# Optimization experiments

Measured on AMD Instinct MI355X. Metric: run time of the kernel, lower is better.

The kernel has to match this reference:

```python
import jax, jax.numpy as jnp
import numpy as np

C, C_LO, C_MF = 96, 32, 32  # c_hf = 96 - 32 - 32 = 32
K_LO, K_HI, LP_FINE, LP_COARSE = 5, 3, 3, 7
BN_EPS = 1e-5


def _avgpool_same(x, k):
    """AvgPool2d(k, stride=1, padding=k//2, count_include_pad=False) on NCHW."""
    p = k // 2
    dims, strides = (1, 1, k, k), (1, 1, 1, 1)
    pads = ((0, 0), (0, 0), (p, p), (p, p))
    s = jax.lax.reduce_window(x, jnp.float32(0), jax.lax.add, dims, strides, pads)
    ones = jnp.ones((1, 1) + x.shape[2:], x.dtype)
    cnt = jax.lax.reduce_window(ones, jnp.float32(0), jax.lax.add, dims, strides, pads)
    return s / cnt  # divide by number of VALID (non-pad) elements


def _dwconv(x, w, k):
    """Depthwise conv, 'same' padding, no bias. w: (C, 1, k, k)."""
    p = k // 2
    return jax.lax.conv_general_dilated(
        x, w, window_strides=(1, 1), padding=((p, p), (p, p)),
        dimension_numbers=("NCHW", "OIHW", "NCHW"),
        feature_group_count=x.shape[1])


def setup_inputs() -> dict:
    key = jax.random.key(0)
    ks = jax.random.split(key, 8)
    B, H, W = 8, 256, 256
    return {
        "x": jax.random.normal(ks[0], (B, C, H, W), jnp.float32),
        "w_lo": jax.random.normal(ks[1], (C_LO, 1, K_LO, K_LO), jnp.float32) * 0.1,
        "w_mf": jax.random.normal(ks[2], (C_MF, 1, 3, 3), jnp.float32) * 0.2,
        "w_hf": jax.random.normal(ks[3], (C - C_LO - C_MF, 1, K_HI, K_HI), jnp.float32) * 0.2,
        "bn_gamma": jax.random.uniform(ks[4], (C,), jnp.float32, 0.5, 1.5),
        "bn_beta": jax.random.normal(ks[5], (C,), jnp.float32) * 0.1,
        "bn_mean": jax.random.normal(ks[6], (C,), jnp.float32) * 0.1,
        "bn_var": jax.random.uniform(ks[7], (C,), jnp.float32, 0.5, 1.5),
    }


def reference(x, w_lo, w_mf, w_hf, bn_gamma, bn_beta, bn_mean, bn_var):
    x_lo = x[:, :C_LO]
    x_mf = x[:, C_LO:C_LO + C_MF]
    x_hf = x[:, C_LO + C_MF:]

    y_lo = _dwconv(x_lo, w_lo, K_LO)
    # band-pass: fine low-pass minus coarse low-pass
    x_mf_bp = _avgpool_same(x_mf, LP_FINE) - _avgpool_same(x_mf, LP_COARSE)
    y_mf = _dwconv(x_mf_bp, w_mf, 3)
    # high-pass: identity minus fine low-pass
    x_hf_hp = x_hf - _avgpool_same(x_hf, LP_FINE)
    y_hf = _dwconv(x_hf_hp, w_hf, K_HI)

    y = jnp.concatenate([y_lo, y_mf, y_hf], axis=1)

    # channel shuffle with groups=3 (C % 3 == 0 here)
    B, Cc, H, W = y.shape
    y = y.reshape(B, 3, Cc // 3, H, W).transpose(0, 2, 1, 3, 4).reshape(B, Cc, H, W)

    # BatchNorm2d (inference mode, running stats) + SiLU
    inv = bn_gamma * jax.lax.rsqrt(bn_var + BN_EPS)
    y = y * inv[None, :, None, None] + (bn_beta - bn_mean * inv)[None, :, None, None]
    return jax.nn.silu(y)
```

## Files before the change

### kernel.cpp

```cpp
#include <hip/hip_runtime.h>

#define HH 256
#define WW 256
#define CC 96
#define BB 8

__device__ __forceinline__ float silu_of(float z) {
    return z / (1.0f + __expf(-z));
}

__global__ __launch_bounds__(256, 4)
void trifreq_kernel(const float* __restrict__ x,
                    const float* __restrict__ w_lo,
                    const float* __restrict__ w_mf,
                    const float* __restrict__ w_hf,
                    const float* __restrict__ gamma,
                    const float* __restrict__ beta,
                    const float* __restrict__ mean,
                    const float* __restrict__ var,
                    float* __restrict__ out)
{
    __shared__ __align__(16) float xs[74 * 72 + 16];
    __shared__ __align__(16) float tmp[68 * 68];

    const int tid = threadIdx.x;
    const int tileIdx = blockIdx.x;
    const int c = blockIdx.y;
    const int b = blockIdx.z;
    const int th = (tileIdx >> 2) * 64;
    const int tw = (tileIdx & 3) * 64;

    const int g = c >> 5;
    const int ci = c & 31;
    const int c_out = ci * 3 + g;

    const float* __restrict__ xin = x + (((size_t)b * CC + c) * (size_t)HH) * (size_t)WW;

    for (int idx = tid; idx < 72 * 18; idx += 256) {
        const int r  = idx / 18;
        const int c4 = idx % 18;
        const int gh = th - 4 + r;
        const int gw = tw - 4 + 4 * c4;
        float4 v = make_float4(0.f, 0.f, 0.f, 0.f);
        if (gh >= 0 && gh < HH && gw >= 0 && gw + 3 < WW) {
            v = *reinterpret_cast<const float4*>(xin + (size_t)gh * WW + gw);
        }
        *reinterpret_cast<float4*>(&xs[r * 72 + 4 * c4]) = v;
    }
    __syncthreads();

    const int qr = (tid >> 4) << 2;
    const int qc = (tid & 15) << 2;
    float acc[4][4];

    if (g == 0) {
        const float* __restrict__ wp = w_lo + ci * 25;
        float wk[25];
        #pragma unroll
        for (int t = 0; t < 25; ++t) wk[t] = wp[t];
        #pragma unroll
        for (int i = 0; i < 4; ++i)
            #pragma unroll
            for (int j = 0; j < 4; ++j) acc[i][j] = 0.f;

        #pragma unroll
        for (int rr = 0; rr < 8; ++rr) {
            const float* row = &xs[(qr + rr + 2) * 72 + qc];
            float v[12];
            *reinterpret_cast<float4*>(&v[0]) = *reinterpret_cast<const float4*>(row);
            *reinterpret_cast<float4*>(&v[4]) = *reinterpret_cast<const float4*>(row + 4);
            *reinterpret_cast<float4*>(&v[8]) = *reinterpret_cast<const float4*>(row + 8);
            #pragma unroll
            for (int i = 0; i < 4; ++i) {
                const int ki = rr - i;
                if (ki >= 0 && ki < 5) {
                    #pragma unroll
                    for (int j = 0; j < 4; ++j)
                        acc[i][j] += v[j + 2] * wk[ki * 5 + 0]
                                   + v[j + 3] * wk[ki * 5 + 1]
                                   + v[j + 4] * wk[ki * 5 + 2]
                                   + v[j + 5] * wk[ki * 5 + 3]
                                   + v[j + 6] * wk[ki * 5 + 4];
                }
            }
        }
    } else {
        if (g == 1) {
            for (int p = tid; p < 17 * 17; p += 256) {
                const int pr = p / 17, pc = p % 17;
                const int br = pr * 4 - 1, bc = pc * 4 - 1;
                float v7a[4][4] = {};
                float v3a[4][4] = {};
                #pragma unroll
                for (int rr = 0; rr < 10; ++rr) {
                    const float* row = &xs[(pr * 4 + rr) * 72 + pc * 4];
                    float v[12];
                    *reinterpret_cast<float4*>(&v[0]) = *reinterpret_cast<const float4*>(row);
                    *reinterpret_cast<float4*>(&v[4]) = *reinterpret_cast<const float4*>(row + 4);
                    *reinterpret_cast<float4*>(&v[8]) = *reinterpret_cast<const float4*>(row + 8);
                    float h7[4], h3[4];
                    float s = v[0] + v[1] + v[2] + v[3] + v[4] + v[5] + v[6];
                    h7[0] = s;
                    h7[1] = h7[0] + v[7] - v[0];
                    h7[2] = h7[1] + v[8] - v[1];
                    h7[3] = h7[2] + v[9] - v[2];
                    #pragma unroll
                    for (int j = 0; j < 4; ++j) h3[j] = v[j + 2] + v[j + 3] + v[j + 4];
                    #pragma unroll
                    for (int k = 0; k < 4; ++k) {
                        if (rr >= k && rr <= k + 6) {
                            #pragma unroll
                            for (int j = 0; j < 4; ++j) v7a[k][j] += h7[j];
                        }
                        if (rr >= k + 2 && rr <= k + 4) {
                            #pragma unroll
                            for (int j = 0; j < 4; ++j) v3a[k][j] += h3[j];
                        }
                    }
                }
                float r3h[4], r7h[4], r3w[4], r7w[4];
                #pragma unroll
                for (int i = 0; i < 4; ++i) {
                    const int hh = th + br + i;
                    const int a3 = min(hh + 1, HH - 1) - max(hh - 1, 0) + 1;
                    const int a7 = min(hh + 3, HH - 1) - max(hh - 3, 0) + 1;
                    r3h[i] = 1.0f / (float)a3;
                    r7h[i] = 1.0f / (float)a7;
                }
                #pragma unroll
                for (int j = 0; j < 4; ++j) {
                    const int ww = tw + bc + j;
                    const int a3 = min(ww + 1, WW - 1) - max(ww - 1, 0) + 1;
                    const int a7 = min(ww + 3, WW - 1) - max(ww - 3, 0) + 1;
                    r3w[j] = 1.0f / (float)a3;
                    r7w[j] = 1.0f / (float)a7;
                }
                #pragma unroll
                for (int i = 0; i < 4; ++i) {
                    const int hh = th + br + i;
                    float bpv[4];
                    #pragma unroll
                    for (int j = 0; j < 4; ++j) {
                        const int ww = tw + bc + j;
                        float bp = 0.f;
                        if (hh >= 0 && hh < HH && ww >= 0 && ww < WW)
                            bp = v3a[i][j] * (r3h[i] * r3w[j]) - v7a[i][j] * (r7h[i] * r7w[j]);
                        bpv[j] = bp;
                    }
                    *reinterpret_cast<float4*>(&tmp[(pr * 4 + i) * 68 + pc * 4]) =
                        make_float4(bpv[0], bpv[1], bpv[2], bpv[3]);
                }
            }
        } else {
            for (int p = tid; p < 17 * 17; p += 256) {
                const int pr = p / 17, pc = p % 17;
                const int br = pr * 4 - 1, bc = pc * 4 - 1;
                float v3a[4][4] = {};
                float cen[4][4];
                #pragma unroll
                for (int rr = 0; rr < 6; ++rr) {
                    const float* row = &xs[(pr * 4 + 2 + rr) * 72 + pc * 4];
                    float v[8];
                    *reinterpret_cast<float4*>(&v[0]) = *reinterpret_cast<const float4*>(row);
                    *reinterpret_cast<float4*>(&v[4]) = *reinterpret_cast<const float4*>(row + 4);
                    float h3[4];
                    #pragma unroll
                    for (int j = 0; j < 4; ++j) h3[j] = v[j + 2] + v[j + 3] + v[j + 4];
                    if (rr >= 1 && rr <= 4) {
                        #pragma unroll
                        for (int j = 0; j < 4; ++j) cen[rr - 1][j] = v[j + 3];
                    }
                    #pragma unroll
                    for (int k = 0; k < 4; ++k) {
                        if (rr >= k && rr <= k + 2) {
                            #pragma unroll
                            for (int j = 0; j < 4; ++j) v3a[k][j] += h3[j];
                        }
                    }
                }
                float r3h[4], r3w[4];
                #pragma unroll
                for (int i = 0; i < 4; ++i) {
                    const int hh = th + br + i;
                    const int a3 = min(hh + 1, HH - 1) - max(hh - 1, 0) + 1;
                    r3h[i] = 1.0f / (float)a3;
                }
                #pragma unroll
                for (int j = 0; j < 4; ++j) {
                    const int ww = tw + bc + j;
                    const int a3 = min(ww + 1, WW - 1) - max(ww - 1, 0) + 1;
                    r3w[j] = 1.0f / (float)a3;
                }
                #pragma unroll
                for (int i = 0; i < 4; ++i) {
                    const int hh = th + br + i;
                    float hpv[4];
                    #pragma unroll
                    for (int j = 0; j < 4; ++j) {
                        const int ww = tw + bc + j;
                        float hp = 0.f;
                        if (hh >= 0 && hh < HH && ww >= 0 && ww < WW)
                            hp = cen[i][j] - v3a[i][j] * (r3h[i] * r3w[j]);
                        hpv[j] = hp;
                    }
                    *reinterpret_cast<float4*>(&tmp[(pr * 4 + i) * 68 + pc * 4]) =
                        make_float4(hpv[0], hpv[1], hpv[2], hpv[3]);
                }
            }
        }
        __syncthreads();

        const float* __restrict__ wp = ((g == 1) ? w_mf : w_hf) + ci * 9;
        float wk[9];
        #pragma unroll
        for (int t = 0; t < 9; ++t) wk[t] = wp[t];
        #pragma unroll
        for (int i = 0; i < 4; ++i)
            #pragma unroll
            for (int j = 0; j < 4; ++j) acc[i][j] = 0.f;

        #pragma unroll
        for (int rr = 0; rr < 6; ++rr) {
            const float* row = &tmp[(qr + rr) * 68 + qc];
            float v[8];
            *reinterpret_cast<float4*>(&v[0]) = *reinterpret_cast<const float4*>(row);
            *reinterpret_cast<float4*>(&v[4]) = *reinterpret_cast<const float4*>(row + 4);
            #pragma unroll
            for (int i = 0; i < 4; ++i) {
                const int ki = rr - i;
                if (ki >= 0 && ki < 3) {
                    #pragma unroll
                    for (int j = 0; j < 4; ++j)
                        acc[i][j] += v[j + 0] * wk[ki * 3 + 0]
                                   + v[j + 1] * wk[ki * 3 + 1]
                                   + v[j + 2] * wk[ki * 3 + 2];
                }
            }
        }
    }

    const float bninv  = gamma[c_out] * rsqrtf(var[c_out] + 1e-5f);
    const float bnbias = beta[c_out] - mean[c_out] * bninv;
    float* __restrict__ op = out + (((size_t)b * CC + c_out) * (size_t)HH + (th + qr)) * (size_t)WW + (tw + qc);
    #pragma unroll
    for (int i = 0; i < 4; ++i) {
        float4 o;
        const float z0 = acc[i][0] * bninv + bnbias;
        const float z1 = acc[i][1] * bninv + bnbias;
        const float z2 = acc[i][2] * bninv + bnbias;
        const float z3 = acc[i][3] * bninv + bnbias;
        o.x = silu_of(z0);
        o.y = silu_of(z1);
        o.z = silu_of(z2);
        o.w = silu_of(z3);
        *reinterpret_cast<float4*>(op + (size_t)i * WW) = o;
    }
}

extern "C" void kernel_launch(void* const* d_in, const int* in_sizes, int n_in,
                              void* d_out, int out_size, void* d_ws, size_t ws_size,
                              hipStream_t stream) {
    const float* x     = (const float*)d_in[0];
    const float* w_lo  = (const float*)d_in[1];
    const float* w_mf  = (const float*)d_in[2];
    const float* w_hf  = (const float*)d_in[3];
    const float* gam   = (const float*)d_in[4];
    const float* bet   = (const float*)d_in[5];
    const float* mea   = (const float*)d_in[6];
    const float* va    = (const float*)d_in[7];
    float* out = (float*)d_out;

    dim3 grid(16, CC, BB);
    dim3 block(256);
    hipLaunchKernelGGL(trifreq_kernel, grid, block, 0, stream,
                       x, w_lo, w_mf, w_hf, gam, bet, mea, va, out);
}
```

Measured before the change: 380.3 us.

## Split filtered intermediate into two row halves to shrink LDS and raise occupancy

The mid and high band paths now build the filtered intermediate in two 32-row halves inside a smaller shared buffer (36x68 instead of 68x68). Each half is convolved and written out before the next, with an extra barrier in between. This cuts LDS per block so launch bounds can target 5 blocks per SIMD. It also fast-paths the average-pool reciprocal counts for interior tiles and hoists the BN constants. In exchange it recomputes halo rows between halves, adds a barrier, and leaves 103 threads idle during the filter phase.

```diff
diff --git a/kernel.cpp b/kernel.cpp
--- a/kernel.cpp
+++ b/kernel.cpp
@@ -9,7 +9,7 @@
     return z / (1.0f + __expf(-z));
 }
 
-__global__ __launch_bounds__(256, 4)
+__global__ __launch_bounds__(256, 5)
 void trifreq_kernel(const float* __restrict__ x,
                     const float* __restrict__ w_lo,
                     const float* __restrict__ w_mf,
@@ -21,7 +21,7 @@
                     float* __restrict__ out)
 {
     __shared__ __align__(16) float xs[74 * 72 + 16];
-    __shared__ __align__(16) float tmp[68 * 68];
+    __shared__ __align__(16) float tmp[36 * 68];
 
     const int tid = threadIdx.x;
     const int tileIdx = blockIdx.x;
@@ -35,6 +35,9 @@
     const int c_out = ci * 3 + g;
 
     const float* __restrict__ xin = x + (((size_t)b * CC + c) * (size_t)HH) * (size_t)WW;
+
+    const float bninv  = gamma[c_out] * rsqrtf(var[c_out] + 1e-5f);
+    const float bnbias = beta[c_out] - mean[c_out] * bninv;
 
     for (int idx = tid; idx < 72 * 18; idx += 256) {
         const int r  = idx / 18;
@@ -49,15 +52,14 @@
     }
     __syncthreads();
 
-    const int qr = (tid >> 4) << 2;
-    const int qc = (tid & 15) << 2;
-    float acc[4][4];
-
     if (g == 0) {
+        const int qr = (tid >> 4) << 2;
+        const int qc = (tid & 15) << 2;
         const float* __restrict__ wp = w_lo + ci * 25;
         float wk[25];
         #pragma unroll
         for (int t = 0; t < 25; ++t) wk[t] = wp[t];
+        float acc[4][4];
         #pragma unroll
         for (int i = 0; i < 4; ++i)
             #pragma unroll
@@ -84,176 +86,215 @@
                 }
             }
         }
+
+        float* __restrict__ op = out + (((size_t)b * CC + c_out) * (size_t)HH + (th + qr)) * (size_t)WW + (tw + qc);
+        #pragma unroll
+        for (int i = 0; i < 4; ++i) {
+            float4 o;
+            o.x = silu_of(acc[i][0] * bninv + bnbias);
+            o.y = silu_of(acc[i][1] * bninv + bnbias);
+            o.z = silu_of(acc[i][2] * bninv + bnbias);
+            o.w = silu_of(acc[i][3] * bninv + bnbias);
+            *reinterpret_cast<float4*>(op + (size_t)i * WW) = o;
+        }
     } else {
-        if (g == 1) {
-            for (int p = tid; p < 17 * 17; p += 256) {
-                const int pr = p / 17, pc = p % 17;
-                const int br = pr * 4 - 1, bc = pc * 4 - 1;
-                float v7a[4][4] = {};
-                float v3a[4][4] = {};
-                #pragma unroll
-                for (int rr = 0; rr < 10; ++rr) {
-                    const float* row = &xs[(pr * 4 + rr) * 72 + pc * 4];
-                    float v[12];
-                    *reinterpret_cast<float4*>(&v[0]) = *reinterpret_cast<const float4*>(row);
-                    *reinterpret_cast<float4*>(&v[4]) = *reinterpret_cast<const float4*>(row + 4);
-                    *reinterpret_cast<float4*>(&v[8]) = *reinterpret_cast<const float4*>(row + 8);
-                    float h7[4], h3[4];
-                    float s = v[0] + v[1] + v[2] + v[3] + v[4] + v[5] + v[6];
-                    h7[0] = s;
-                    h7[1] = h7[0] + v[7] - v[0];
-                    h7[2] = h7[1] + v[8] - v[1];
-                    h7[3] = h7[2] + v[9] - v[2];
-                    #pragma unroll
-                    for (int j = 0; j < 4; ++j) h3[j] = v[j + 2] + v[j + 3] + v[j + 4];
-                    #pragma unroll
-                    for (int k = 0; k < 4; ++k) {
-                        if (rr >= k && rr <= k + 6) {
+        const float* __restrict__ wp = ((g == 1) ? w_mf : w_hf) + ci * 9;
+        float wk[9];
+        #pragma unroll
+        for (int t = 0; t < 9; ++t) wk[t] = wp[t];
+
+        for (int c0 = 0; c0 < 2; ++c0) {
+            const int R0 = c0 * 32 - 1;
+
+            if (tid < 153) {
+                int pr, pc;
+                if (tid < 144) { pr = tid >> 4; pc = tid & 15; }
+                else           { pr = tid - 144; pc = 16; }
+                const int bc = pc * 4 - 1;
+                const int hb = th + R0 + pr * 4;
+                const int wb = tw + bc;
+
+                if (g == 1) {
+                    const int xrb = R0 + 1 + pr * 4;
+                    float v7a[4][4] = {};
+                    float v3a[4][4] = {};
+                    #pragma unroll
+                    for (int rr = 0; rr < 10; ++rr) {
+                        const float* row = &xs[(xrb + rr) * 72 + pc * 4];
+                        float v[12];
+                        *reinterpret_cast<float4*>(&v[0]) = *reinterpret_cast<const float4*>(row);
+                        *reinterpret_cast<float4*>(&v[4]) = *reinterpret_cast<const float4*>(row + 4);
+                        *reinterpret_cast<float4*>(&v[8]) = *reinterpret_cast<const float4*>(row + 8);
+                        float h7[4], h3[4];
+                        float s = v[0] + v[1] + v[2] + v[3] + v[4] + v[5] + v[6];
+                        h7[0] = s;
+                        h7[1] = h7[0] + v[7] - v[0];
+                        h7[2] = h7[1] + v[8] - v[1];
+                        h7[3] = h7[2] + v[9] - v[2];
+                        #pragma unroll
+                        for (int j = 0; j < 4; ++j) h3[j] = v[j + 2] + v[j + 3] + v[j + 4];
+                        #pragma unroll
+                        for (int k = 0; k < 4; ++k) {
+                            if (rr >= k && rr <= k + 6) {
+                                #pragma unroll
+                                for (int j = 0; j < 4; ++j) v7a[k][j] += h7[j];
+                            }
+                            if (rr >= k + 2 && rr <= k + 4) {
+                                #pragma unroll
+                                for (int j = 0; j < 4; ++j) v3a[k][j] += h3[j];
+                            }
+                        }
+                    }
+                    float r3h[4], r7h[4], r3w[4], r7w[4];
+                    if (hb >= 3 && hb + 6 <= HH - 1) {
+                        #pragma unroll
+                        for (int i = 0; i < 4; ++i) { r3h[i] = (1.f / 3.f); r7h[i] = (1.f / 7.f); }
+                    } else {
+                        #pragma unroll
+                        for (int i = 0; i < 4; ++i) {
+                            const int hh = hb + i;
+                            const int a3 = min(hh + 1, HH - 1) - max(hh - 1, 0) + 1;
+                            const int a7 = min(hh + 3, HH - 1) - max(hh - 3, 0) + 1;
+                            r3h[i] = 1.0f / (float)a3;
+                            r7h[i] = 1.0f / (float)a7;
+                        }
+                    }
+                    if (wb >= 3 && wb + 6 <= WW - 1) {
+                        #pragma unroll
+                        for (int j = 0; j < 4; ++j) { r3w[j] = (1.f / 3.f); r7w[j] = (1.f / 7.f); }
+                    } else {
+                        #pragma unroll
+                        for (int j = 0; j < 4; ++j) {
+                            const int ww = wb + j;
+                            const int a3 = min(ww + 1, WW - 1) - max(ww - 1, 0) + 1;
+                            const int a7 = min(ww + 3, WW - 1) - max(ww - 3, 0) + 1;
+                            r3w[j] = 1.0f / (float)a3;
+                            r7w[j] = 1.0f / (float)a7;
+                        }
+                    }
+                    #pragma unroll
+                    for (int i = 0; i < 4; ++i) {
+                        const int hh = hb + i;
+                        float bpv[4];
+                        #pragma unroll
+                        for (int j = 0; j < 4; ++j) {
+                            const int ww = wb + j;
+                            float bp = 0.f;
+                            if (hh >= 0 && hh < HH && ww >= 0 && ww < WW)
+                                bp = v3a[i][j] * (r3h[i] * r3w[j]) - v7a[i][j] * (r7h[i] * r7w[j]);
+                            bpv[j] = bp;
+                        }
+                        *reinterpret_cast<float4*>(&tmp[(pr * 4 + i) * 68 + pc * 4]) =
+                            make_float4(bpv[0], bpv[1], bpv[2], bpv[3]);
+                    }
+                } else {
+                    const int xrb = R0 + 3 + pr * 4;
+                    float v3a[4][4] = {};
+                    float cen[4][4];
+                    #pragma unroll
+                    for (int rr = 0; rr < 6; ++rr) {
+                        const float* row = &xs[(xrb + rr) * 72 + pc * 4];
+                        float v[8];
+                        *reinterpret_cast<float4*>(&v[0]) = *reinterpret_cast<const float4*>(row);
+                        *reinterpret_cast<float4*>(&v[4]) = *reinterpret_cast<const float4*>(row + 4);
+                        float h3[4];
+                        #pragma unroll
+                        for (int j = 0; j < 4; ++j) h3[j] = v[j + 2] + v[j + 3] + v[j + 4];
+                        if (rr >= 1 && rr <= 4) {
                             #pragma unroll
-                            for (int j = 0; j < 4; ++j) v7a[k][j] += h7[j];
-                        }
-                        if (rr >= k + 2 && rr <= k + 4) {
-                            #pragma unroll
-                            for (int j = 0; j < 4; ++j) v3a[k][j] += h3[j];
-                        }
-                    }
-                }
-                float r3h[4], r7h[4], r3w[4], r7w[4];
-                #pragma unroll
-                for (int i = 0; i < 4; ++i) {
-                    const int hh = th + br + i;
-                    const int a3 = min(hh + 1, HH - 1) - max(hh - 1, 0) + 1;
-                    const int a7 = min(hh + 3, HH - 1) - max(hh - 3, 0) + 1;
-                    r3h[i] = 1.0f / (float)a3;
-                    r7h[i] = 1.0f / (float)a7;
-                }
-                #pragma unroll
-                for (int j = 0; j < 4; ++j) {
-                    const int ww = tw + bc + j;
-                    const int a3 = min(ww + 1, WW - 1) - max(ww - 1, 0) + 1;
-                    const int a7 = min(ww + 3, WW - 1) - max(ww - 3, 0) + 1;
-                    r3w[j] = 1.0f / (float)a3;
-                    r7w[j] = 1.0f / (float)a7;
-                }
-                #pragma unroll
-                for (int i = 0; i < 4; ++i) {
-                    const int hh = th + br + i;
-                    float bpv[4];
-                    #pragma unroll
-                    for (int j = 0; j < 4; ++j) {
-                        const int ww = tw + bc + j;
-                        float bp = 0.f;
-                        if (hh >= 0 && hh < HH && ww >= 0 && ww < WW)
-                            bp = v3a[i][j] * (r3h[i] * r3w[j]) - v7a[i][j] * (r7h[i] * r7w[j]);
-                        bpv[j] = bp;
-                    }
-                    *reinterpret_cast<float4*>(&tmp[(pr * 4 + i) * 68 + pc * 4]) =
-                        make_float4(bpv[0], bpv[1], bpv[2], bpv[3]);
+                            for (int j = 0; j < 4; ++j) cen[rr - 1][j] = v[j + 3];
+                        }
+                        #pragma unroll
+                        for (int k = 0; k < 4; ++k) {
+                            if (rr >= k && rr <= k + 2) {
+                                #pragma unroll
+                                for (int j = 0; j < 4; ++j) v3a[k][j] += h3[j];
+                            }
+                        }
+                    }
+                    float r3h[4], r3w[4];
+                    if (hb >= 1 && hb + 4 <= HH - 1) {
+                        #pragma unroll
+                        for (int i = 0; i < 4; ++i) r3h[i] = (1.f / 3.f);
+                    } else {
+                        #pragma unroll
+                        for (int i = 0; i < 4; ++i) {
+                            const int hh = hb + i;
+                            const int a3 = min(hh + 1, HH - 1) - max(hh - 1, 0) + 1;
+                            r3h[i] = 1.0f / (float)a3;
+                        }
+                    }
+                    if (wb >= 1 && wb + 4 <= WW - 1) {
+                        #pragma unroll
+                        for (int j = 0; j < 4; ++j) r3w[j] = (1.f / 3.f);
+                    } else {
+                        #pragma unroll
+                        for (int j = 0; j < 4; ++j) {
+                            const int ww = wb + j;
+                            const int a3 = min(ww + 1, WW - 1) - max(ww - 1, 0) + 1;
+                            r3w[j] = 1.0f / (float)a3;
+                        }
+                    }
+                    #pragma unroll
+                    for (int i = 0; i < 4; ++i) {
+                        const int hh = hb + i;
+                        float hpv[4];
+                        #pragma unroll
+                        for (int j = 0; j < 4; ++j) {
+                            const int ww = wb + j;
+                            float hp = 0.f;
+                            if (hh >= 0 && hh < HH && ww >= 0 && ww < WW)
+                                hp = cen[i][j] - v3a[i][j] * (r3h[i] * r3w[j]);
+                            hpv[j] = hp;
+                        }
+                        *reinterpret_cast<float4*>(&tmp[(pr * 4 + i) * 68 + pc * 4]) =
+                            make_float4(hpv[0], hpv[1], hpv[2], hpv[3]);
+                    }
                 }
             }
-        } else {
-            for (int p = tid; p < 17 * 17; p += 256) {
-                const int pr = p / 17, pc = p % 17;
-                const int br = pr * 4 - 1, bc = pc * 4 - 1;
-                float v3a[4][4] = {};
-                float cen[4][4];
+            __syncthreads();
+
+            const int lqr = (tid >> 4) * 2;
+            const int qc  = (tid & 15) * 4;
+            float acc2[2][4];
+            #pragma unroll
+            for (int i = 0; i < 2; ++i)
                 #pragma unroll
-                for (int rr = 0; rr < 6; ++rr) {
-                    const float* row = &xs[(pr * 4 + 2 + rr) * 72 + pc * 4];
-                    float v[8];
-                    *reinterpret_cast<float4*>(&v[0]) = *reinterpret_cast<const float4*>(row);
-                    *reinterpret_cast<float4*>(&v[4]) = *reinterpret_cast<const float4*>(row + 4);
-                    float h3[4];
-                    #pragma unroll
-                    for (int j = 0; j < 4; ++j) h3[j] = v[j + 2] + v[j + 3] + v[j + 4];
-                    if (rr >= 1 && rr <= 4) {
-                        #pragma unroll
-                        for (int j = 0; j < 4; ++j) cen[rr - 1][j] = v[j + 3];
-                    }
-                    #pragma unroll
-                    for (int k = 0; k < 4; ++k) {
-                        if (rr >= k && rr <= k + 2) {
-                            #pragma unroll
-                            for (int j = 0; j < 4; ++j) v3a[k][j] += h3[j];
-                        }
-                    }
-                }
-                float r3h[4], r3w[4];
+                for (int j = 0; j < 4; ++j) acc2[i][j] = 0.f;
+
+            #pragma unroll
+            for (int rr = 0; rr < 4; ++rr) {
+                const float* row = &tmp[(lqr + rr) * 68 + qc];
+                float v[8];
+                *reinterpret_cast<float4*>(&v[0]) = *reinterpret_cast<const float4*>(row);
+                *reinterpret_cast<float4*>(&v[4]) = *reinterpret_cast<const float4*>(row + 4);
                 #pragma unroll
-                for (int i = 0; i < 4; ++i) {
-                    const int hh = th + br + i;
-                    const int a3 = min(hh + 1, HH - 1) - max(hh - 1, 0) + 1;
-                    r3h[i] = 1.0f / (float)a3;
-                }
-                #pragma unroll
-                for (int j = 0; j < 4; ++j) {
-                    const int ww = tw + bc + j;
-                    const int a3 = min(ww + 1, WW - 1) - max(ww - 1, 0) + 1;
-                    r3w[j] = 1.0f / (float)a3;
-                }
-                #pragma unroll
-                for (int i = 0; i < 4; ++i) {
-                    const int hh = th + br + i;
-                    float hpv[4];
-                    #pragma unroll
-                    for (int j = 0; j < 4; ++j) {
-                        const int ww = tw + bc + j;
-                        float hp = 0.f;
-                        if (hh >= 0 && hh < HH && ww >= 0 && ww < WW)
-                            hp = cen[i][j] - v3a[i][j] * (r3h[i] * r3w[j]);
-                        hpv[j] = hp;
-                    }
-                    *reinterpret_cast<float4*>(&tmp[(pr * 4 + i) * 68 + pc * 4]) =
-                        make_float4(hpv[0], hpv[1], hpv[2], hpv[3]);
+                for (int i = 0; i < 2; ++i) {
+                    const int ki = rr - i;
+                    if (ki >= 0 && ki < 3) {
+                        #pragma unroll
+                        for (int j = 0; j < 4; ++j)
+                            acc2[i][j] += v[j + 0] * wk[ki * 3 + 0]
+                                        + v[j + 1] * wk[ki * 3 + 1]
+                                        + v[j + 2] * wk[ki * 3 + 2];
+                    }
                 }
             }
+
+            float* __restrict__ op = out + (((size_t)b * CC + c_out) * (size_t)HH
+                                            + (th + c0 * 32 + lqr)) * (size_t)WW + (tw + qc);
+            #pragma unroll
+            for (int i = 0; i < 2; ++i) {
+                float4 o;
+                o.x = silu_of(acc2[i][0] * bninv + bnbias);
+                o.y = silu_of(acc2[i][1] * bninv + bnbias);
+                o.z = silu_of(acc2[i][2] * bninv + bnbias);
+                o.w = silu_of(acc2[i][3] * bninv + bnbias);
+                *reinterpret_cast<float4*>(op + (size_t)i * WW) = o;
+            }
+
+            if (c0 == 0) __syncthreads();
         }
-        __syncthreads();
-
-        const float* __restrict__ wp = ((g == 1) ? w_mf : w_hf) + ci * 9;
-        float wk[9];
-        #pragma unroll
-        for (int t = 0; t < 9; ++t) wk[t] = wp[t];
-        #pragma unroll
-        for (int i = 0; i < 4; ++i)
-            #pragma unroll
-            for (int j = 0; j < 4; ++j) acc[i][j] = 0.f;
-
-        #pragma unroll
-        for (int rr = 0; rr < 6; ++rr) {
-            const float* row = &tmp[(qr + rr) * 68 + qc];
-            float v[8];
-            *reinterpret_cast<float4*>(&v[0]) = *reinterpret_cast<const float4*>(row);
-            *reinterpret_cast<float4*>(&v[4]) = *reinterpret_cast<const float4*>(row + 4);
-            #pragma unroll
-            for (int i = 0; i < 4; ++i) {
-                const int ki = rr - i;
-                if (ki >= 0 && ki < 3) {
-                    #pragma unroll
-                    for (int j = 0; j < 4; ++j)
-                        acc[i][j] += v[j + 0] * wk[ki * 3 + 0]
-                                   + v[j + 1] * wk[ki * 3 + 1]
-                                   + v[j + 2] * wk[ki * 3 + 2];
-                }
-            }
-        }
-    }
-
-    const float bninv  = gamma[c_out] * rsqrtf(var[c_out] + 1e-5f);
-    const float bnbias = beta[c_out] - mean[c_out] * bninv;
-    float* __restrict__ op = out + (((size_t)b * CC + c_out) * (size_t)HH + (th + qr)) * (size_t)WW + (tw + qc);
-    #pragma unroll
-    for (int i = 0; i < 4; ++i) {
-        float4 o;
-        const float z0 = acc[i][0] * bninv + bnbias;
-        const float z1 = acc[i][1] * bninv + bnbias;
-        const float z2 = acc[i][2] * bninv + bnbias;
-        const float z3 = acc[i][3] * bninv + bnbias;
-        o.x = silu_of(z0);
-        o.y = silu_of(z1);
-        o.z = silu_of(z2);
-        o.w = silu_of(z3);
-        *reinterpret_cast<float4*>(op + (size_t)i * WW) = o;
     }
 }
 
```

Measured after the change: 505.6 us. 1.33x slower.

## Loop each block over four column tiles with register-prefetched next tile

Applied to the files above, without the earlier changes.

Each block now handles a full 64-row strip and walks four 64-column tiles. The next tile's input is loaded into registers before the current tile is computed, then written to shared memory after a barrier. The aim is to hide global load latency behind compute and amortise the BN parameter loads. In exchange the grid is four times smaller (about 3072 blocks), and the extra float4 registers plus added barriers may lower occupancy. Tile halos are still reloaded from global memory rather than reused.

```diff
diff --git a/kernel.cpp b/kernel.cpp
--- a/kernel.cpp
+++ b/kernel.cpp
@@ -23,24 +23,26 @@
     __shared__ __align__(16) float xs[74 * 72 + 16];
     __shared__ __align__(16) float tmp[68 * 68];
 
-    const int tid = threadIdx.x;
-    const int tileIdx = blockIdx.x;
-    const int c = blockIdx.y;
-    const int b = blockIdx.z;
-    const int th = (tileIdx >> 2) * 64;
-    const int tw = (tileIdx & 3) * 64;
-
-    const int g = c >> 5;
+    const int tid  = threadIdx.x;
+    const int trow = blockIdx.x;
+    const int c    = blockIdx.y;
+    const int b    = blockIdx.z;
+    const int th   = trow * 64;
+
+    const int g  = c >> 5;
     const int ci = c & 31;
     const int c_out = ci * 3 + g;
 
     const float* __restrict__ xin = x + (((size_t)b * CC + c) * (size_t)HH) * (size_t)WW;
+
+    const float bninv  = gamma[c_out] * rsqrtf(var[c_out] + 1e-5f);
+    const float bnbias = beta[c_out] - mean[c_out] * bninv;
 
     for (int idx = tid; idx < 72 * 18; idx += 256) {
         const int r  = idx / 18;
         const int c4 = idx % 18;
         const int gh = th - 4 + r;
-        const int gw = tw - 4 + 4 * c4;
+        const int gw = -4 + 4 * c4;
         float4 v = make_float4(0.f, 0.f, 0.f, 0.f);
         if (gh >= 0 && gh < HH && gw >= 0 && gw + 3 < WW) {
             v = *reinterpret_cast<const float4*>(xin + (size_t)gh * WW + gw);
@@ -49,211 +51,242 @@
     }
     __syncthreads();
 
-    const int qr = (tid >> 4) << 2;
-    const int qc = (tid & 15) << 2;
-    float acc[4][4];
-
-    if (g == 0) {
-        const float* __restrict__ wp = w_lo + ci * 25;
-        float wk[25];
-        #pragma unroll
-        for (int t = 0; t < 25; ++t) wk[t] = wp[t];
-        #pragma unroll
-        for (int i = 0; i < 4; ++i)
-            #pragma unroll
-            for (int j = 0; j < 4; ++j) acc[i][j] = 0.f;
-
-        #pragma unroll
-        for (int rr = 0; rr < 8; ++rr) {
-            const float* row = &xs[(qr + rr + 2) * 72 + qc];
-            float v[12];
-            *reinterpret_cast<float4*>(&v[0]) = *reinterpret_cast<const float4*>(row);
-            *reinterpret_cast<float4*>(&v[4]) = *reinterpret_cast<const float4*>(row + 4);
-            *reinterpret_cast<float4*>(&v[8]) = *reinterpret_cast<const float4*>(row + 8);
-            #pragma unroll
-            for (int i = 0; i < 4; ++i) {
-                const int ki = rr - i;
-                if (ki >= 0 && ki < 5) {
-                    #pragma unroll
-                    for (int j = 0; j < 4; ++j)
-                        acc[i][j] += v[j + 2] * wk[ki * 5 + 0]
-                                   + v[j + 3] * wk[ki * 5 + 1]
-                                   + v[j + 4] * wk[ki * 5 + 2]
-                                   + v[j + 5] * wk[ki * 5 + 3]
-                                   + v[j + 6] * wk[ki * 5 + 4];
-                }
-            }
-        }
-    } else {
-        if (g == 1) {
-            for (int p = tid; p < 17 * 17; p += 256) {
-                const int pr = p / 17, pc = p % 17;
-                const int br = pr * 4 - 1, bc = pc * 4 - 1;
-                float v7a[4][4] = {};
-                float v3a[4][4] = {};
+    for (int tc = 0; tc < 4; ++tc) {
+        const int tw = tc * 64;
+
+        float4 pf[6];
+        if (tc < 3) {
+            const int tw2 = tw + 64;
+            #pragma unroll
+            for (int k = 0; k < 6; ++k) {
+                const int idx = tid + (k << 8);
+                const int r  = idx / 18;
+                const int c4 = idx % 18;
+                const int gh = th - 4 + r;
+                const int gw = tw2 - 4 + 4 * c4;
+                float4 v = make_float4(0.f, 0.f, 0.f, 0.f);
+                if (idx < 1296 && gh >= 0 && gh < HH && gw >= 0 && gw + 3 < WW) {
+                    v = *reinterpret_cast<const float4*>(xin + (size_t)gh * WW + gw);
+                }
+                pf[k] = v;
+            }
+        }
+
+        const int qr = (tid >> 4) << 2;
+        const int qc = (tid & 15) << 2;
+        float acc[4][4];
+
+        if (g == 0) {
+            const float* __restrict__ wp = w_lo + ci * 25;
+            float wk[25];
+            #pragma unroll
+            for (int t = 0; t < 25; ++t) wk[t] = wp[t];
+            #pragma unroll
+            for (int i = 0; i < 4; ++i)
                 #pragma unroll
-                for (int rr = 0; rr < 10; ++rr) {
-                    const float* row = &xs[(pr * 4 + rr) * 72 + pc * 4];
-                    float v[12];
-                    *reinterpret_cast<float4*>(&v[0]) = *reinterpret_cast<const float4*>(row);
-                    *reinterpret_cast<float4*>(&v[4]) = *reinterpret_cast<const float4*>(row + 4);
-                    *reinterpret_cast<float4*>(&v[8]) = *reinterpret_cast<const float4*>(row + 8);
-                    float h7[4], h3[4];
-                    float s = v[0] + v[1] + v[2] + v[3] + v[4] + v[5] + v[6];
-                    h7[0] = s;
-                    h7[1] = h7[0] + v[7] - v[0];
-                    h7[2] = h7[1] + v[8] - v[1];
-                    h7[3] = h7[2] + v[9] - v[2];
-                    #pragma unroll
-                    for (int j = 0; j < 4; ++j) h3[j] = v[j + 2] + v[j + 3] + v[j + 4];
-                    #pragma unroll
-                    for (int k = 0; k < 4; ++k) {
-                        if (rr >= k && rr <= k + 6) {
-                            #pragma unroll
-                            for (int j = 0; j < 4; ++j) v7a[k][j] += h7[j];
-                        }
-                        if (rr >= k + 2 && rr <= k + 4) {
-                            #pragma unroll
-                            for (int j = 0; j < 4; ++j) v3a[k][j] += h3[j];
-                        }
-                    }
-                }
-                float r3h[4], r7h[4], r3w[4], r7w[4];
+                for (int j = 0; j < 4; ++j) acc[i][j] = 0.f;
+
+            #pragma unroll
+            for (int rr = 0; rr < 8; ++rr) {
+                const float* row = &xs[(qr + rr + 2) * 72 + qc];
+                float v[12];
+                *reinterpret_cast<float4*>(&v[0]) = *reinterpret_cast<const float4*>(row);
+                *reinterpret_cast<float4*>(&v[4]) = *reinterpret_cast<const float4*>(row + 4);
+                *reinterpret_cast<float4*>(&v[8]) = *reinterpret_cast<const float4*>(row + 8);
                 #pragma unroll
                 for (int i = 0; i < 4; ++i) {
-                    const int hh = th + br + i;
-                    const int a3 = min(hh + 1, HH - 1) - max(hh - 1, 0) + 1;
-                    const int a7 = min(hh + 3, HH - 1) - max(hh - 3, 0) + 1;
-                    r3h[i] = 1.0f / (float)a3;
-                    r7h[i] = 1.0f / (float)a7;
-                }
+                    const int ki = rr - i;
+                    if (ki >= 0 && ki < 5) {
+                        #pragma unroll
+                        for (int j = 0; j < 4; ++j)
+                            acc[i][j] += v[j + 2] * wk[ki * 5 + 0]
+                                       + v[j + 3] * wk[ki * 5 + 1]
+                                       + v[j + 4] * wk[ki * 5 + 2]
+                                       + v[j + 5] * wk[ki * 5 + 3]
+                                       + v[j + 6] * wk[ki * 5 + 4];
+                    }
+                }
+            }
+        } else {
+            if (g == 1) {
+                for (int p = tid; p < 17 * 17; p += 256) {
+                    const int pr = p / 17, pc = p % 17;
+                    const int br = pr * 4 - 1, bc = pc * 4 - 1;
+                    float v7a[4][4] = {};
+                    float v3a[4][4] = {};
+                    #pragma unroll
+                    for (int rr = 0; rr < 10; ++rr) {
+                        const float* row = &xs[(pr * 4 + rr) * 72 + pc * 4];
+                        float v[12];
+                        *reinterpret_cast<float4*>(&v[0]) = *reinterpret_cast<const float4*>(row);
+                        *reinterpret_cast<float4*>(&v[4]) = *reinterpret_cast<const float4*>(row + 4);
+                        *reinterpret_cast<float4*>(&v[8]) = *reinterpret_cast<const float4*>(row + 8);
+                        float h7[4], h3[4];
+                        float s = v[0] + v[1] + v[2] + v[3] + v[4] + v[5] + v[6];
+                        h7[0] = s;
+                        h7[1] = h7[0] + v[7] - v[0];
+                        h7[2] = h7[1] + v[8] - v[1];
+                        h7[3] = h7[2] + v[9] - v[2];
+                        #pragma unroll
+                        for (int j = 0; j < 4; ++j) h3[j] = v[j + 2] + v[j + 3] + v[j + 4];
+                        #pragma unroll
+                        for (int k = 0; k < 4; ++k) {
+                            if (rr >= k && rr <= k + 6) {
+                                #pragma unroll
+                                for (int j = 0; j < 4; ++j) v7a[k][j] += h7[j];
+                            }
+                            if (rr >= k + 2 && rr <= k + 4) {
+                                #pragma unroll
+                                for (int j = 0; j < 4; ++j) v3a[k][j] += h3[j];
+                            }
+                        }
+                    }
+                    float r3h[4], r7h[4], r3w[4], r7w[4];
+                    #pragma unroll
+                    for (int i = 0; i < 4; ++i) {
+                        const int hh = th + br + i;
+                        const int a3 = min(hh + 1, HH - 1) - max(hh - 1, 0) + 1;
+                        const int a7 = min(hh + 3, HH - 1) - max(hh - 3, 0) + 1;
+                        r3h[i] = 1.0f / (float)a3;
+                        r7h[i] = 1.0f / (float)a7;
+                    }
+                    #pragma unroll
+                    for (int j = 0; j < 4; ++j) {
+                        const int ww = tw + bc + j;
+                        const int a3 = min(ww + 1, WW - 1) - max(ww - 1, 0) + 1;
+                        const int a7 = min(ww + 3, WW - 1) - max(ww - 3, 0) + 1;
+                        r3w[j] = 1.0f / (float)a3;
+                        r7w[j] = 1.0f / (float)a7;
+                    }
+                    #pragma unroll
+                    for (int i = 0; i < 4; ++i) {
+                        const int hh = th + br + i;
+                        float bpv[4];
+                        #pragma unroll
+                        for (int j = 0; j < 4; ++j) {
+                            const int ww = tw + bc + j;
+                            float bp = 0.f;
+                            if (hh >= 0 && hh < HH && ww >= 0 && ww < WW)
+                                bp = v3a[i][j] * (r3h[i] * r3w[j]) - v7a[i][j] * (r7h[i] * r7w[j]);
+                            bpv[j] = bp;
+                        }
+                        *reinterpret_cast<float4*>(&tmp[(pr * 4 + i) * 68 + pc * 4]) =
+                            make_float4(bpv[0], bpv[1], bpv[2], bpv[3]);
+                    }
+                }
+            } else {
+                for (int p = tid; p < 17 * 17; p += 256) {
+                    const int pr = p / 17, pc = p % 17;
+                    const int br = pr * 4 - 1, bc = pc * 4 - 1;
+                    float v3a[4][4] = {};
+                    float cen[4][4];
+                    #pragma unroll
+                    for (int rr = 0; rr < 6; ++rr) {
+                        const float* row = &xs[(pr * 4 + 2 + rr) * 72 + pc * 4];
+                        float v[8];
+                        *reinterpret_cast<float4*>(&v[0]) = *reinterpret_cast<const float4*>(row);
+                        *reinterpret_cast<float4*>(&v[4]) = *reinterpret_cast<const float4*>(row + 4);
+                        float h3[4];
+                        #pragma unroll
+                        for (int j = 0; j < 4; ++j) h3[j] = v[j + 2] + v[j + 3] + v[j + 4];
+                        if (rr >= 1 && rr <= 4) {
+                            #pragma unroll
+                            for (int j = 0; j < 4; ++j) cen[rr - 1][j] = v[j + 3];
+                        }
+                        #pragma unroll
+                        for (int k = 0; k < 4; ++k) {
+                            if (rr >= k && rr <= k + 2) {
+                                #pragma unroll
+                                for (int j = 0; j < 4; ++j) v3a[k][j] += h3[j];
+                            }
+                        }
+                    }
+                    float r3h[4], r3w[4];
+                    #pragma unroll
+                    for (int i = 0; i < 4; ++i) {
+                        const int hh = th + br + i;
+                        const int a3 = min(hh + 1, HH - 1) - max(hh - 1, 0) + 1;
+                        r3h[i] = 1.0f / (float)a3;
+                    }
+                    #pragma unroll
+                    for (int j = 0; j < 4; ++j) {
+                        const int ww = tw + bc + j;
+                        const int a3 = min(ww + 1, WW - 1) - max(ww - 1, 0) + 1;
+                        r3w[j] = 1.0f / (float)a3;
+                    }
+                    #pragma unroll
+                    for (int i = 0; i < 4; ++i) {
+                        const int hh = th + br + i;
+                        float hpv[4];
+                        #pragma unroll
+                        for (int j = 0; j < 4; ++j) {
+                            const int ww = tw + bc + j;
+                            float hp = 0.f;
+                            if (hh >= 0 && hh < HH && ww >= 0 && ww < WW)
+                                hp = cen[i][j] - v3a[i][j] * (r3h[i] * r3w[j]);
+                            hpv[j] = hp;
+                        }
+                        *reinterpret_cast<float4*>(&tmp[(pr * 4 + i) * 68 + pc * 4]) =
+                            make_float4(hpv[0], hpv[1], hpv[2], hpv[3]);
+                    }
+                }
+            }
+            __syncthreads();
+
+            const float* __restrict__ wp = ((g == 1) ? w_mf : w_hf) + ci * 9;
+            float wk[9];
+            #pragma unroll
+            for (int t = 0; t < 9; ++t) wk[t] = wp[t];
+            #pragma unroll
+            for (int i = 0; i < 4; ++i)
                 #pragma unroll
-                for (int j = 0; j < 4; ++j) {
-                    const int ww = tw + bc + j;
-                    const int a3 = min(ww + 1, WW - 1) - max(ww - 1, 0) + 1;
-                    const int a7 = min(ww + 3, WW - 1) - max(ww - 3, 0) + 1;
-                    r3w[j] = 1.0f / (float)a3;
-                    r7w[j] = 1.0f / (float)a7;
-                }
+                for (int j = 0; j < 4; ++j) acc[i][j] = 0.f;
+
+            #pragma unroll
+            for (int rr = 0; rr < 6; ++rr) {
+                const float* row = &tmp[(qr + rr) * 68 + qc];
+                float v[8];
+                *reinterpret_cast<float4*>(&v[0]) = *reinterpret_cast<const float4*>(row);
+                *reinterpret_cast<float4*>(&v[4]) = *reinterpret_cast<const float4*>(row + 4);
                 #pragma unroll
                 for (int i = 0; i < 4; ++i) {
-                    const int hh = th + br + i;
-                    float bpv[4];
-                    #pragma unroll
-                    for (int j = 0; j < 4; ++j) {
-                        const int ww = tw + bc + j;
-                        float bp = 0.f;
-                        if (hh >= 0 && hh < HH && ww >= 0 && ww < WW)
-                            bp = v3a[i][j] * (r3h[i] * r3w[j]) - v7a[i][j] * (r7h[i] * r7w[j]);
-                        bpv[j] = bp;
-                    }
-                    *reinterpret_cast<float4*>(&tmp[(pr * 4 + i) * 68 + pc * 4]) =
-                        make_float4(bpv[0], bpv[1], bpv[2], bpv[3]);
-                }
-            }
-        } else {
-            for (int p = tid; p < 17 * 17; p += 256) {
-                const int pr = p / 17, pc = p % 17;
-                const int br = pr * 4 - 1, bc = pc * 4 - 1;
-                float v3a[4][4] = {};
-                float cen[4][4];
-                #pragma unroll
-                for (int rr = 0; rr < 6; ++rr) {
-                    const float* row = &xs[(pr * 4 + 2 + rr) * 72 + pc * 4];
-                    float v[8];
-                    *reinterpret_cast<float4*>(&v[0]) = *reinterpret_cast<const float4*>(row);
-                    *reinterpret_cast<float4*>(&v[4]) = *reinterpret_cast<const float4*>(row + 4);
-                    float h3[4];
-                    #pragma unroll
-                    for (int j = 0; j < 4; ++j) h3[j] = v[j + 2] + v[j + 3] + v[j + 4];
-                    if (rr >= 1 && rr <= 4) {
-                        #pragma unroll
-                        for (int j = 0; j < 4; ++j) cen[rr - 1][j] = v[j + 3];
-                    }
-                    #pragma unroll
-                    for (int k = 0; k < 4; ++k) {
-                        if (rr >= k && rr <= k + 2) {
-                            #pragma unroll
-                            for (int j = 0; j < 4; ++j) v3a[k][j] += h3[j];
-                        }
-                    }
-                }
-                float r3h[4], r3w[4];
-                #pragma unroll
-                for (int i = 0; i < 4; ++i) {
-                    const int hh = th + br + i;
-                    const int a3 = min(hh + 1, HH - 1) - max(hh - 1, 0) + 1;
-                    r3h[i] = 1.0f / (float)a3;
-                }
-                #pragma unroll
-                for (int j = 0; j < 4; ++j) {
-                    const int ww = tw + bc + j;
-                    const int a3 = min(ww + 1, WW - 1) - max(ww - 1, 0) + 1;
-                    r3w[j] = 1.0f / (float)a3;
-                }
-                #pragma unroll
-                for (int i = 0; i < 4; ++i) {
-                    const int hh = th + br + i;
-                    float hpv[4];
-                    #pragma unroll
-                    for (int j = 0; j < 4; ++j) {
-                        const int ww = tw + bc + j;
-                        float hp = 0.f;
-                        if (hh >= 0 && hh < HH && ww >= 0 && ww < WW)
-                            hp = cen[i][j] - v3a[i][j] * (r3h[i] * r3w[j]);
-                        hpv[j] = hp;
-                    }
-                    *reinterpret_cast<float4*>(&tmp[(pr * 4 + i) * 68 + pc * 4]) =
-                        make_float4(hpv[0], hpv[1], hpv[2], hpv[3]);
-                }
-            }
-        }
-        __syncthreads();
-
-        const float* __restrict__ wp = ((g == 1) ? w_mf : w_hf) + ci * 9;
-        float wk[9];
+                    const int ki = rr - i;
+                    if (ki >= 0 && ki < 3) {
+                        #pragma unroll
+                        for (int j = 0; j < 4; ++j)
+                            acc[i][j] += v[j + 0] * wk[ki * 3 + 0]
+                                       + v[j + 1] * wk[ki * 3 + 1]
+                                       + v[j + 2] * wk[ki * 3 + 2];
+                    }
+                }
+            }
+        }
+
+        float* __restrict__ op = out + (((size_t)b * CC + c_out) * (size_t)HH + (th + qr)) * (size_t)WW + (tw + qc);
         #pragma unroll
-        for (int t = 0; t < 9; ++t) wk[t] = wp[t];
-        #pragma unroll
-        for (int i = 0; i < 4; ++i)
-            #pragma unroll
-            for (int j = 0; j < 4; ++j) acc[i][j] = 0.f;
-
-        #pragma unroll
-        for (int rr = 0; rr < 6; ++rr) {
-            const float* row = &tmp[(qr + rr) * 68 + qc];
-            float v[8];
-            *reinterpret_cast<float4*>(&v[0]) = *reinterpret_cast<const float4*>(row);
-            *reinterpret_cast<float4*>(&v[4]) = *reinterpret_cast<const float4*>(row + 4);
-            #pragma unroll
-            for (int i = 0; i < 4; ++i) {
-                const int ki = rr - i;
-                if (ki >= 0 && ki < 3) {
-                    #pragma unroll
-                    for (int j = 0; j < 4; ++j)
-                        acc[i][j] += v[j + 0] * wk[ki * 3 + 0]
-                                   + v[j + 1] * wk[ki * 3 + 1]
-                                   + v[j + 2] * wk[ki * 3 + 2];
-                }
-            }
-        }
-    }
-
-    const float bninv  = gamma[c_out] * rsqrtf(var[c_out] + 1e-5f);
-    const float bnbias = beta[c_out] - mean[c_out] * bninv;
-    float* __restrict__ op = out + (((size_t)b * CC + c_out) * (size_t)HH + (th + qr)) * (size_t)WW + (tw + qc);
-    #pragma unroll
-    for (int i = 0; i < 4; ++i) {
-        float4 o;
-        const float z0 = acc[i][0] * bninv + bnbias;
-        const float z1 = acc[i][1] * bninv + bnbias;
-        const float z2 = acc[i][2] * bninv + bnbias;
-        const float z3 = acc[i][3] * bninv + bnbias;
-        o.x = silu_of(z0);
-        o.y = silu_of(z1);
-        o.z = silu_of(z2);
-        o.w = silu_of(z3);
-        *reinterpret_cast<float4*>(op + (size_t)i * WW) = o;
+        for (int i = 0; i < 4; ++i) {
+            float4 o;
+            o.x = silu_of(acc[i][0] * bninv + bnbias);
+            o.y = silu_of(acc[i][1] * bninv + bnbias);
+            o.z = silu_of(acc[i][2] * bninv + bnbias);
+            o.w = silu_of(acc[i][3] * bninv + bnbias);
+            *reinterpret_cast<float4*>(op + (size_t)i * WW) = o;
+        }
+
+        if (tc < 3) {
+            if (g == 0) __syncthreads();
+            else        __syncthreads();
+            #pragma unroll
+            for (int k = 0; k < 6; ++k) {
+                const int idx = tid + (k << 8);
+                if (idx < 1296) {
+                    const int r  = idx / 18;
+                    const int c4 = idx % 18;
+                    *reinterpret_cast<float4*>(&xs[r * 72 + 4 * c4]) = pf[k];
+                }
+            }
+            __syncthreads();
+        }
     }
 }
 
@@ -270,7 +303,7 @@
     const float* va    = (const float*)d_in[7];
     float* out = (float*)d_out;
 
-    dim3 grid(16, CC, BB);
+    dim3 grid(4, CC, BB);
     dim3 block(256);
     hipLaunchKernelGGL(trifreq_kernel, grid, block, 0, stream,
                        x, w_lo, w_mf, w_hf, gam, bet, mea, va, out);
```

Result: slower. 562.7 us (+48.0%).
